# Kernel tuning notes

Hardware: AMD Instinct MI355X
Metric: run time of the kernel (lower is better)

Reference implementation:

```python
import jax, jax.numpy as jnp
import numpy as np

NEG_SLOPE = 0.01  # torch nn.LeakyReLU default


def setup_inputs() -> dict:
    key = jax.random.key(0)
    k1, k2, k3, k4, k5 = jax.random.split(key, 5)
    B, C, N, O = 32, 512, 1024, 512
    x = jax.random.normal(k1, (B, C, N), dtype=jnp.float32)
    wq = jax.random.normal(k2, (C,), dtype=jnp.float32) * (1.0 / np.sqrt(C))
    wk = jax.random.normal(k3, (C,), dtype=jnp.float32) * (1.0 / np.sqrt(C))
    wm = jax.random.normal(k4, (O, C), dtype=jnp.float32) * (1.0 / np.sqrt(C))
    bm = jax.random.normal(k5, (O,), dtype=jnp.float32) * 0.01
    return {"x": x, "wq": wq, "wk": wk, "wm": wm, "bm": bm}


def reference(x, wq, wk, wm, bm):
    # x: [B, C, N]
    q = jnp.einsum('c,bcn->bn', wq, x)            # [B, N] (Conv1d C->1, k=1, no bias)
    k = jnp.einsum('c,bcn->bn', wk, x)            # [B, N]
    scores = q[:, None, :] + k[:, :, None]        # [B, N, N] additive broadcast
    scores = jnp.where(scores > 0, scores, NEG_SLOPE * scores)  # LeakyReLU
    att = jax.nn.softmax(scores, axis=-1)         # softmax over last dim
    agg = jnp.einsum('bcn,bmn->bcm', x, att)      # weighted aggregation [B, C, N]
    out = jnp.einsum('oc,bcm->bom', wm, agg) + bm[None, :, None]  # Conv1d k=1
    return jax.nn.relu(out)
```

## Files before the change

kernel.cpp:

```cpp
#include <hip/hip_runtime.h>


constexpr int B = 32, C = 512, N = 1024, O = 512;
constexpr float L2E = 1.4426950408889634f;

typedef _Float16 half8 __attribute__((ext_vector_type(8)));
typedef _Float16 half4v __attribute__((ext_vector_type(4)));
typedef _Float16 half2v __attribute__((ext_vector_type(2)));
typedef float f32x4 __attribute__((ext_vector_type(4)));

#if __has_builtin(__builtin_amdgcn_exp2f)
#define EXP2(x) __builtin_amdgcn_exp2f(x)
#else
#define EXP2(x) exp2f(x)
#endif

__device__ __forceinline__ half8 cvt8(float4 a, float4 b) {
  half8 h;
  h[0] = (_Float16)a.x; h[1] = (_Float16)a.y; h[2] = (_Float16)a.z; h[3] = (_Float16)a.w;
  h[4] = (_Float16)b.x; h[5] = (_Float16)b.y; h[6] = (_Float16)b.z; h[7] = (_Float16)b.w;
  return h;
}

__device__ __forceinline__ unsigned fenc(float x) {
  unsigned u = __float_as_uint(x);
  return (u & 0x80000000u) ? ~u : (u ^ 0x80000000u);
}
__device__ __forceinline__ float fdec(unsigned e) {
  unsigned u = (e & 0x80000000u) ? (e ^ 0x80000000u) : ~e;
  return __uint_as_float(u);
}

__global__ __launch_bounds__(256) void gemm_y_kernel(const float* __restrict__ x,
    const float* __restrict__ wm, const float* __restrict__ wq,
    const float* __restrict__ wk, float* __restrict__ q, float* __restrict__ k,
    unsigned* __restrict__ qmax_u, _Float16* __restrict__ Yt) {
  __shared__ half2v Xs[16 * 130];
  __shared__ __align__(16) _Float16 Ws[128 * 40];
  __shared__ float mred[4];
  int b  = blockIdx.y;
  int n0 = blockIdx.x * 128;
  int o0 = blockIdx.z * 128;
  int t = threadIdx.x;
  int w = t >> 6, l = t & 63;
  int nw = w >> 1, ow = w & 1;
  int lm = l & 15, q8 = (l >> 4) * 8, q4 = (l >> 4) * 4;

  int cp = t >> 4, ng = t & 15;
  int wrow = t >> 2, woff = (t & 3) * 8;
  bool doqk = (blockIdx.z == 0);
  float aq[8] = {}, ak[8] = {};

  f32x4 acc[4][4] = {};
  for (int c0 = 0; c0 < C; c0 += 32) {
    const float* xr = x + ((size_t)b * C + c0 + 2 * cp) * N + n0 + ng * 8;
    float4 a0 = *(const float4*)(xr);
    float4 a1 = *(const float4*)(xr + 4);
    float4 b0 = *(const float4*)(xr + N);
    float4 b1 = *(const float4*)(xr + N + 4);
    const float* wr = wm + (size_t)(o0 + wrow) * C + c0 + woff;
    float4 w0 = *(const float4*)(wr);
    float4 w1 = *(const float4*)(wr + 4);
    float4 w2 = *(const float4*)(wr + (size_t)64 * C);
    float4 w3 = *(const float4*)(wr + (size_t)64 * C + 4);

    if (doqk) {
      float2 wq2 = *(const float2*)&wq[c0 + 2 * cp];
      float2 wk2 = *(const float2*)&wk[c0 + 2 * cp];
      aq[0] = fmaf(wq2.x, a0.x, fmaf(wq2.y, b0.x, aq[0]));
      aq[1] = fmaf(wq2.x, a0.y, fmaf(wq2.y, b0.y, aq[1]));
      aq[2] = fmaf(wq2.x, a0.z, fmaf(wq2.y, b0.z, aq[2]));
      aq[3] = fmaf(wq2.x, a0.w, fmaf(wq2.y, b0.w, aq[3]));
      aq[4] = fmaf(wq2.x, a1.x, fmaf(wq2.y, b1.x, aq[4]));
      aq[5] = fmaf(wq2.x, a1.y, fmaf(wq2.y, b1.y, aq[5]));
      aq[6] = fmaf(wq2.x, a1.z, fmaf(wq2.y, b1.z, aq[6]));
      aq[7] = fmaf(wq2.x, a1.w, fmaf(wq2.y, b1.w, aq[7]));
      ak[0] = fmaf(wk2.x, a0.x, fmaf(wk2.y, b0.x, ak[0]));
      ak[1] = fmaf(wk2.x, a0.y, fmaf(wk2.y, b0.y, ak[1]));
      ak[2] = fmaf(wk2.x, a0.z, fmaf(wk2.y, b0.z, ak[2]));
      ak[3] = fmaf(wk2.x, a0.w, fmaf(wk2.y, b0.w, ak[3]));
      ak[4] = fmaf(wk2.x, a1.x, fmaf(wk2.y, b1.x, ak[4]));
      ak[5] = fmaf(wk2.x, a1.y, fmaf(wk2.y, b1.y, ak[5]));
      ak[6] = fmaf(wk2.x, a1.z, fmaf(wk2.y, b1.z, ak[6]));
      ak[7] = fmaf(wk2.x, a1.w, fmaf(wk2.y, b1.w, ak[7]));
    }

    __syncthreads();
    {
      half2v* xp = &Xs[cp * 130 + ng * 8];
      xp[0] = half2v{(_Float16)a0.x, (_Float16)b0.x};
      xp[1] = half2v{(_Float16)a0.y, (_Float16)b0.y};
      xp[2] = half2v{(_Float16)a0.z, (_Float16)b0.z};
      xp[3] = half2v{(_Float16)a0.w, (_Float16)b0.w};
      xp[4] = half2v{(_Float16)a1.x, (_Float16)b1.x};
      xp[5] = half2v{(_Float16)a1.y, (_Float16)b1.y};
      xp[6] = half2v{(_Float16)a1.z, (_Float16)b1.z};
      xp[7] = half2v{(_Float16)a1.w, (_Float16)b1.w};
      *(half8*)&Ws[wrow * 40 + woff]        = cvt8(w0, w1);
      *(half8*)&Ws[(wrow + 64) * 40 + woff] = cvt8(w2, w3);
    }
    __syncthreads();

    half8 af[4], bf[4];
#pragma unroll
    for (int i = 0; i < 4; ++i) {
      int nrow = nw * 64 + i * 16 + lm;
#pragma unroll
      for (int jp = 0; jp < 4; ++jp) {
        half2v p = Xs[(q4 + jp) * 130 + nrow];
        af[i][2 * jp]     = p[0];
        af[i][2 * jp + 1] = p[1];
      }
    }
#pragma unroll
    for (int j = 0; j < 4; ++j)
      bf[j] = *(const half8*)&Ws[(ow * 64 + j * 16 + lm) * 40 + q8];
#pragma unroll
    for (int i = 0; i < 4; ++i)
#pragma unroll
      for (int j = 0; j < 4; ++j)
        acc[i][j] = __builtin_amdgcn_mfma_f32_16x16x32_f16(af[i], bf[j], acc[i][j], 0, 0, 0);
  }

#pragma unroll
  for (int i = 0; i < 4; ++i) {
    int n_b = n0 + nw * 64 + i * 16 + (l >> 4) * 4;
#pragma unroll
    for (int j = 0; j < 4; ++j) {
      int o_c = o0 + ow * 64 + j * 16 + lm;
      half4v h;
      h[0] = (_Float16)acc[i][j][0];
      h[1] = (_Float16)acc[i][j][1];
      h[2] = (_Float16)acc[i][j][2];
      h[3] = (_Float16)acc[i][j][3];
      *(half4v*)&Yt[((size_t)b * O + o_c) * N + n_b] = h;
    }
  }

  if (doqk) {
    float* red = (float*)Ws;
    float qv_final = -1e30f;
    __syncthreads();
#pragma unroll
    for (int j = 0; j < 8; ++j) red[cp * 132 + ng * 8 + j] = aq[j];
    __syncthreads();
    if (t < 128) {
      float s = 0.f;
#pragma unroll
      for (int p = 0; p < 16; ++p) s += red[p * 132 + t];
      qv_final = L2E * s;
      q[b * N + n0 + t] = qv_final;
    }
    __syncthreads();
#pragma unroll
    for (int j = 0; j < 8; ++j) red[cp * 132 + ng * 8 + j] = ak[j];
    __syncthreads();
    if (t < 128) {
      float s = 0.f;
#pragma unroll
      for (int p = 0; p < 16; ++p) s += red[p * 132 + t];
      k[b * N + n0 + t] = L2E * s;
    }
    float m = qv_final;
#pragma unroll
    for (int off = 32; off > 0; off >>= 1) m = fmaxf(m, __shfl_down(m, off, 64));
    if ((t & 63) == 0) mred[t >> 6] = m;
    __syncthreads();
    if (t == 0) {
      float bmax = fmaxf(fmaxf(mred[0], mred[1]), fmaxf(mred[2], mred[3]));
      atomicMax(&qmax_u[b], fenc(bmax));
    }
  }
}

__global__ __launch_bounds__(256) void gemm_out_kernel(const _Float16* __restrict__ Yt,
    const float* __restrict__ q, const float* __restrict__ k,
    const unsigned* __restrict__ qmax_u, const float* __restrict__ bm,
    float* __restrict__ out) {
  __shared__ __align__(16) float qs[N];
  __shared__ __align__(16) _Float16 Ys[2][128 * 40];
  __shared__ float izs[128];
  int b  = blockIdx.y;
  int o0 = blockIdx.x * 128;
  int m0 = blockIdx.z * 128;
  int t = threadIdx.x;
  int w = t >> 6, l = t & 63;
  int lm = l & 15, g = l >> 4, q8 = g * 8;

  *(float4*)&qs[t * 4] = *(const float4*)&q[b * N + t * 4];

  float qmv = fdec(qmax_u[b]);
  float k2[2], k3[2];
#pragma unroll
  for (int i = 0; i < 2; ++i) {
    float km = k[b * N + m0 + w * 32 + i * 16 + lm];
    float s0 = qmv + km;
    float M  = fmaxf(s0, 0.01f * s0);
    k2[i] = km - M;
    k3[i] = fmaf(0.01f, km, -M);
  }
  float Zp[2] = {0.f, 0.f};
  int yr = t >> 1, yp = t & 1;
  const _Float16* ysrc = Yt + ((size_t)b * O + o0 + yr) * N + yp * 16;

  {
    half8 y0 = *(const half8*)(ysrc);
    half8 y1 = *(const half8*)(ysrc + 8);
    *(half8*)&Ys[0][yr * 40 + yp * 16]     = y0;
    *(half8*)&Ys[0][yr * 40 + yp * 16 + 8] = y1;
  }
  __syncthreads();

  f32x4 acc[2][8] = {};
  for (int it = 0; it < N / 32; ++it) {
    int p = it & 1;
    int n0k = it * 32;
    half8 z0, z1;
    if (it < N / 32 - 1) {
      z0 = *(const half8*)(ysrc + n0k + 32);
      z1 = *(const half8*)(ysrc + n0k + 40);
    }
    float4 qa = *(const float4*)&qs[n0k + q8];
    float4 qb = *(const float4*)&qs[n0k + q8 + 4];
    float qv[8] = {qa.x, qa.y, qa.z, qa.w, qb.x, qb.y, qb.z, qb.w};
    half8 af[2];
#pragma unroll
    for (int i = 0; i < 2; ++i) {
      float zz = 0.f;
#pragma unroll
      for (int jj = 0; jj < 8; ++jj) {
        float arg = fmaxf(qv[jj] + k2[i], fmaf(0.01f, qv[jj], k3[i]));
        _Float16 eh = (_Float16)EXP2(arg);
        af[i][jj] = eh;
        zz += (float)eh;
      }
      Zp[i] += zz;
    }
    half8 bf[8];
#pragma unroll
    for (int j = 0; j < 8; ++j)
      bf[j] = *(const half8*)&Ys[p][(j * 16 + lm) * 40 + q8];
#pragma unroll
    for (int i = 0; i < 2; ++i)
#pragma unroll
      for (int j = 0; j < 8; ++j)
        acc[i][j] = __builtin_amdgcn_mfma_f32_16x16x32_f16(af[i], bf[j], acc[i][j], 0, 0, 0);
    if (it < N / 32 - 1) {
      *(half8*)&Ys[p ^ 1][yr * 40 + yp * 16]     = z0;
      *(half8*)&Ys[p ^ 1][yr * 40 + yp * 16 + 8] = z1;
    }
    __syncthreads();
  }

#pragma unroll
  for (int i = 0; i < 2; ++i) {
    float z = Zp[i];
    z += __shfl_xor(z, 16, 64);
    z += __shfl_xor(z, 32, 64);
    if (g == 0) izs[w * 32 + i * 16 + lm] = 1.0f / z;
  }
  __syncthreads();

  float iz4v[2][4];
#pragma unroll
  for (int i = 0; i < 2; ++i) {
    float4 iz4 = *(const float4*)&izs[w * 32 + i * 16 + g * 4];
    iz4v[i][0] = iz4.x; iz4v[i][1] = iz4.y; iz4v[i][2] = iz4.z; iz4v[i][3] = iz4.w;
  }
#pragma unroll
  for (int j = 0; j < 8; ++j) {
    int o_c = o0 + j * 16 + lm;
    float bias = bm[o_c];
#pragma unroll
    for (int i = 0; i < 2; ++i) {
      int m_b = m0 + w * 32 + i * 16 + g * 4;
      float4 r;
      r.x = fmaxf(fmaf(acc[i][j][0], iz4v[i][0], bias), 0.f);
      r.y = fmaxf(fmaf(acc[i][j][1], iz4v[i][1], bias), 0.f);
      r.z = fmaxf(fmaf(acc[i][j][2], iz4v[i][2], bias), 0.f);
      r.w = fmaxf(fmaf(acc[i][j][3], iz4v[i][3], bias), 0.f);
      *(float4*)&out[((size_t)b * O + o_c) * N + m_b] = r;
    }
  }
}

extern "C" void kernel_launch(void* const* d_in, const int* in_sizes, int n_in,
                              void* d_out, int out_size, void* d_ws, size_t ws_size,
                              hipStream_t stream) {
  const float* x  = (const float*)d_in[0];
  const float* wq = (const float*)d_in[1];
  const float* wk = (const float*)d_in[2];
  const float* wm = (const float*)d_in[3];
  const float* bm = (const float*)d_in[4];
  float* out = (float*)d_out;

  float* q    = (float*)d_ws;
  float* k    = q + B * N;
  unsigned* qmax_u = (unsigned*)(k + B * N);
  _Float16* Yt = (_Float16*)(qmax_u + 64);

  hipMemsetAsync(qmax_u, 0, 64 * sizeof(unsigned), stream);
  gemm_y_kernel<<<dim3(N / 128, B, O / 128), 256, 0, stream>>>(x, wm, wq, wk, q, k, qmax_u, Yt);
  gemm_out_kernel<<<dim3(O / 128, B, N / 128), 256, 0, stream>>>(Yt, q, k, qmax_u, bm, out);
}
```

Measured before the change: 227.3 us.

## Pre-convert weights to fp16, load MFMA operands directly, and compute softmax sums via MFMA

Adds a small kernel that converts wm to fp16 once per call, so gemm_y loads B fragments straight from global memory instead of staging them through shared memory. This removes the Ws LDS buffer and its writes. In gemm_out, the Y tile double buffer becomes a single buffer with two barriers per iteration. The softmax denominator is now accumulated by an MFMA against a vector of ones instead of scalar adds and shuffles. The risks are extra barriers and lost load/compute overlap in gemm_out, plus one more kernel launch.

```diff
diff --git a/kernel.cpp b/kernel.cpp
--- a/kernel.cpp
+++ b/kernel.cpp
@@ -31,12 +31,19 @@
   return __uint_as_float(u);
 }
 
+__global__ __launch_bounds__(256) void wmh_kernel(const float* __restrict__ wm,
+                                                  _Float16* __restrict__ wmh) {
+  int i = (blockIdx.x * 256 + threadIdx.x) * 8;
+  float4 a = *(const float4*)(wm + i);
+  float4 b = *(const float4*)(wm + i + 4);
+  *(half8*)(wmh + i) = cvt8(a, b);
+}
+
 __global__ __launch_bounds__(256) void gemm_y_kernel(const float* __restrict__ x,
-    const float* __restrict__ wm, const float* __restrict__ wq,
+    const _Float16* __restrict__ wmh, const float* __restrict__ wq,
     const float* __restrict__ wk, float* __restrict__ q, float* __restrict__ k,
     unsigned* __restrict__ qmax_u, _Float16* __restrict__ Yt) {
   __shared__ half2v Xs[16 * 130];
-  __shared__ __align__(16) _Float16 Ws[128 * 40];
   __shared__ float mred[4];
   int b  = blockIdx.y;
   int n0 = blockIdx.x * 128;
@@ -47,9 +54,13 @@
   int lm = l & 15, q8 = (l >> 4) * 8, q4 = (l >> 4) * 4;
 
   int cp = t >> 4, ng = t & 15;
-  int wrow = t >> 2, woff = (t & 3) * 8;
   bool doqk = (blockIdx.z == 0);
   float aq[8] = {}, ak[8] = {};
+
+  const _Float16* wb[4];
+#pragma unroll
+  for (int j = 0; j < 4; ++j)
+    wb[j] = wmh + (size_t)(o0 + ow * 64 + j * 16 + lm) * C + q8;
 
   f32x4 acc[4][4] = {};
   for (int c0 = 0; c0 < C; c0 += 32) {
@@ -58,11 +69,9 @@
     float4 a1 = *(const float4*)(xr + 4);
     float4 b0 = *(const float4*)(xr + N);
     float4 b1 = *(const float4*)(xr + N + 4);
-    const float* wr = wm + (size_t)(o0 + wrow) * C + c0 + woff;
-    float4 w0 = *(const float4*)(wr);
-    float4 w1 = *(const float4*)(wr + 4);
-    float4 w2 = *(const float4*)(wr + (size_t)64 * C);
-    float4 w3 = *(const float4*)(wr + (size_t)64 * C + 4);
+    half8 bf[4];
+#pragma unroll
+    for (int j = 0; j < 4; ++j) bf[j] = *(const half8*)(wb[j] + c0);
 
     if (doqk) {
       float2 wq2 = *(const float2*)&wq[c0 + 2 * cp];
@@ -96,12 +105,10 @@
       xp[5] = half2v{(_Float16)a1.y, (_Float16)b1.y};
       xp[6] = half2v{(_Float16)a1.z, (_Float16)b1.z};
       xp[7] = half2v{(_Float16)a1.w, (_Float16)b1.w};
-      *(half8*)&Ws[wrow * 40 + woff]        = cvt8(w0, w1);
-      *(half8*)&Ws[(wrow + 64) * 40 + woff] = cvt8(w2, w3);
-    }
-    __syncthreads();
-
-    half8 af[4], bf[4];
+    }
+    __syncthreads();
+
+    half8 af[4];
 #pragma unroll
     for (int i = 0; i < 4; ++i) {
       int nrow = nw * 64 + i * 16 + lm;
@@ -112,9 +119,6 @@
         af[i][2 * jp + 1] = p[1];
       }
     }
-#pragma unroll
-    for (int j = 0; j < 4; ++j)
-      bf[j] = *(const half8*)&Ws[(ow * 64 + j * 16 + lm) * 40 + q8];
 #pragma unroll
     for (int i = 0; i < 4; ++i)
 #pragma unroll
@@ -138,27 +142,27 @@
   }
 
   if (doqk) {
-    float* red = (float*)Ws;
+    float* red = (float*)Xs;
     float qv_final = -1e30f;
     __syncthreads();
 #pragma unroll
-    for (int j = 0; j < 8; ++j) red[cp * 132 + ng * 8 + j] = aq[j];
+    for (int j = 0; j < 8; ++j) red[cp * 130 + ng * 8 + j] = aq[j];
     __syncthreads();
     if (t < 128) {
       float s = 0.f;
 #pragma unroll
-      for (int p = 0; p < 16; ++p) s += red[p * 132 + t];
+      for (int p = 0; p < 16; ++p) s += red[p * 130 + t];
       qv_final = L2E * s;
       q[b * N + n0 + t] = qv_final;
     }
     __syncthreads();
 #pragma unroll
-    for (int j = 0; j < 8; ++j) red[cp * 132 + ng * 8 + j] = ak[j];
+    for (int j = 0; j < 8; ++j) red[cp * 130 + ng * 8 + j] = ak[j];
     __syncthreads();
     if (t < 128) {
       float s = 0.f;
 #pragma unroll
-      for (int p = 0; p < 16; ++p) s += red[p * 132 + t];
+      for (int p = 0; p < 16; ++p) s += red[p * 130 + t];
       k[b * N + n0 + t] = L2E * s;
     }
     float m = qv_final;
@@ -178,7 +182,7 @@
     const unsigned* __restrict__ qmax_u, const float* __restrict__ bm,
     float* __restrict__ out) {
   __shared__ __align__(16) float qs[N];
-  __shared__ __align__(16) _Float16 Ys[2][128 * 40];
+  __shared__ __align__(16) _Float16 Ys[128 * 40];
   __shared__ float izs[128];
   int b  = blockIdx.y;
   int o0 = blockIdx.x * 128;
@@ -199,65 +203,54 @@
     k2[i] = km - M;
     k3[i] = fmaf(0.01f, km, -M);
   }
-  float Zp[2] = {0.f, 0.f};
+  half8 ones;
+#pragma unroll
+  for (int jj = 0; jj < 8; ++jj) ones[jj] = (_Float16)1.0f;
+  f32x4 acc_z[2] = {};
   int yr = t >> 1, yp = t & 1;
   const _Float16* ysrc = Yt + ((size_t)b * O + o0 + yr) * N + yp * 16;
-
-  {
-    half8 y0 = *(const half8*)(ysrc);
-    half8 y1 = *(const half8*)(ysrc + 8);
-    *(half8*)&Ys[0][yr * 40 + yp * 16]     = y0;
-    *(half8*)&Ys[0][yr * 40 + yp * 16 + 8] = y1;
-  }
   __syncthreads();
 
   f32x4 acc[2][8] = {};
-  for (int it = 0; it < N / 32; ++it) {
-    int p = it & 1;
-    int n0k = it * 32;
-    half8 z0, z1;
-    if (it < N / 32 - 1) {
-      z0 = *(const half8*)(ysrc + n0k + 32);
-      z1 = *(const half8*)(ysrc + n0k + 40);
-    }
+  for (int n0k = 0; n0k < N; n0k += 32) {
+    half8 y0 = *(const half8*)(ysrc + n0k);
+    half8 y1 = *(const half8*)(ysrc + n0k + 8);
     float4 qa = *(const float4*)&qs[n0k + q8];
     float4 qb = *(const float4*)&qs[n0k + q8 + 4];
     float qv[8] = {qa.x, qa.y, qa.z, qa.w, qb.x, qb.y, qb.z, qb.w};
     half8 af[2];
 #pragma unroll
     for (int i = 0; i < 2; ++i) {
-      float zz = 0.f;
 #pragma unroll
       for (int jj = 0; jj < 8; ++jj) {
         float arg = fmaxf(qv[jj] + k2[i], fmaf(0.01f, qv[jj], k3[i]));
-        _Float16 eh = (_Float16)EXP2(arg);
-        af[i][jj] = eh;
-        zz += (float)eh;
+        af[i][jj] = (_Float16)EXP2(arg);
       }
-      Zp[i] += zz;
-    }
+      acc_z[i] = __builtin_amdgcn_mfma_f32_16x16x32_f16(af[i], ones, acc_z[i], 0, 0, 0);
+    }
+    __syncthreads();
+    *(half8*)&Ys[yr * 40 + yp * 16]     = y0;
+    *(half8*)&Ys[yr * 40 + yp * 16 + 8] = y1;
+    __syncthreads();
+
     half8 bf[8];
 #pragma unroll
     for (int j = 0; j < 8; ++j)
-      bf[j] = *(const half8*)&Ys[p][(j * 16 + lm) * 40 + q8];
+      bf[j] = *(const half8*)&Ys[(j * 16 + lm) * 40 + q8];
 #pragma unroll
     for (int i = 0; i < 2; ++i)
 #pragma unroll
       for (int j = 0; j < 8; ++j)
         acc[i][j] = __builtin_amdgcn_mfma_f32_16x16x32_f16(af[i], bf[j], acc[i][j], 0, 0, 0);
-    if (it < N / 32 - 1) {
-      *(half8*)&Ys[p ^ 1][yr * 40 + yp * 16]     = z0;
-      *(half8*)&Ys[p ^ 1][yr * 40 + yp * 16 + 8] = z1;
-    }
-    __syncthreads();
-  }
-
-#pragma unroll
-  for (int i = 0; i < 2; ++i) {
-    float z = Zp[i];
-    z += __shfl_xor(z, 16, 64);
-    z += __shfl_xor(z, 32, 64);
-    if (g == 0) izs[w * 32 + i * 16 + lm] = 1.0f / z;
+  }
+
+  if (lm == 0) {
+#pragma unroll
+    for (int i = 0; i < 2; ++i) {
+#pragma unroll
+      for (int r = 0; r < 4; ++r)
+        izs[w * 32 + i * 16 + g * 4 + r] = 1.0f / acc_z[i][r];
+    }
   }
   __syncthreads();
 
@@ -297,9 +290,11 @@
   float* q    = (float*)d_ws;
   float* k    = q + B * N;
   unsigned* qmax_u = (unsigned*)(k + B * N);
-  _Float16* Yt = (_Float16*)(qmax_u + 64);
+  _Float16* wmh = (_Float16*)(qmax_u + 64);
+  _Float16* Yt  = wmh + (size_t)O * C;
 
   hipMemsetAsync(qmax_u, 0, 64 * sizeof(unsigned), stream);
-  gemm_y_kernel<<<dim3(N / 128, B, O / 128), 256, 0, stream>>>(x, wm, wq, wk, q, k, qmax_u, Yt);
+  wmh_kernel<<<dim3(O * C / (256 * 8)), 256, 0, stream>>>(wm, wmh);
+  gemm_y_kernel<<<dim3(N / 128, B, O / 128), 256, 0, stream>>>(x, wmh, wq, wk, q, k, qmax_u, Yt);
   gemm_out_kernel<<<dim3(O / 128, B, N / 128), 256, 0, stream>>>(Yt, q, k, qmax_u, bm, out);
 }
```

After: 216.3 us. -4.9%, faster.
